# Kernel optimization log

Hardware: AMD Instinct MI355X
Metric: run time of the kernel (lower is better)

The kernel has to match this reference:

```python
import jax, jax.numpy as jnp
import numpy as np
from jax import lax

K = 3
PAD = 1

def setup_inputs() -> dict:
    key = jax.random.key(0)
    ks = jax.random.split(key, 5)
    B, C, H, W, O = 4, 128, 128, 128, 256
    x = jax.random.normal(ks[0], (B, C, H, W), dtype=jnp.float32)
    w_off = jax.random.normal(ks[1], (3 * K * K, C, K, K), dtype=jnp.float32) * 0.05
    b_off = jnp.zeros((3 * K * K,), dtype=jnp.float32)
    w_dw = jax.random.normal(ks[2], (C, 1, K, K), dtype=jnp.float32) * 0.2
    b_dw = jnp.zeros((C,), dtype=jnp.float32)
    w_pw = jax.random.normal(ks[3], (O, C), dtype=jnp.float32) * (1.0 / np.sqrt(C))
    b_pw = jnp.zeros((O,), dtype=jnp.float32)
    return {"x": x, "w_off": w_off, "b_off": b_off, "w_dw": w_dw,
            "b_dw": b_dw, "w_pw": w_pw, "b_pw": b_pw}

def _dcn_forward(x, w_off, b_off, w_dw, b_dw, w_pw, b_pw):
    B, C, H, W = x.shape
    K2 = K * K
    # offset/mask conv (stride 1, pad 1) -> [B, 3*K*K, H, W]
    om = lax.conv_general_dilated(
        x, w_off, window_strides=(1, 1), padding=[(PAD, PAD), (PAD, PAD)],
        dimension_numbers=("NCHW", "OIHW", "NCHW")) + b_off[None, :, None, None]
    off = om[:, : 2 * K2]                      # [B, 2*K2, H, W]
    mask = jax.nn.sigmoid(om[:, 2 * K2:])      # [B, K2, H, W]
    dy = off[:, 0::2]                          # [B, K2, H, W] (y offsets)
    dx = off[:, 1::2]                          # [B, K2, H, W] (x offsets)
    # base sampling grid per kernel tap
    ky, kx = jnp.meshgrid(jnp.arange(K), jnp.arange(K), indexing="ij")
    ky = (ky.reshape(-1) - PAD).astype(x.dtype)   # [K2]
    kx = (kx.reshape(-1) - PAD).astype(x.dtype)
    py = jnp.arange(H, dtype=x.dtype)[None, None, :, None] + ky[None, :, None, None] + dy
    px = jnp.arange(W, dtype=x.dtype)[None, None, None, :] + kx[None, :, None, None] + dx
    y0 = jnp.floor(py); x0 = jnp.floor(px)
    wy = py - y0;       wx = px - x0

    def gather(yc, xc):
        # yc, xc: [B, K2, H, W] float corner coords; zero outside bounds
        valid = ((yc >= 0) & (yc < H) & (xc >= 0) & (xc < W)).astype(x.dtype)
        yi = jnp.clip(yc, 0, H - 1).astype(jnp.int32)
        xi = jnp.clip(xc, 0, W - 1).astype(jnp.int32)
        idx = yi * W + xi                       # [B, K2, H, W]
        def per_b(xb, ib):
            # xb: [C, H, W]; ib: [K2, H, W] -> [C, K2, H, W]
            return jnp.take(xb.reshape(C, -1), ib.reshape(-1), axis=1).reshape(C, K2, H, W)
        v = jax.vmap(per_b)(x, idx)             # [B, C, K2, H, W]
        return v * valid[:, None]

    val = (gather(y0, x0) * ((1 - wy) * (1 - wx))[:, None]
           + gather(y0, x0 + 1) * ((1 - wy) * wx)[:, None]
           + gather(y0 + 1, x0) * (wy * (1 - wx))[:, None]
           + gather(y0 + 1, x0 + 1) * (wy * wx)[:, None])  # [B, C, K2, H, W]
    val = val * mask[:, None]
    # depthwise deformable conv: per-channel K2 weights
    wk = w_dw.reshape(C, K2)
    out = jnp.einsum("bckhw,ck->bchw", val, wk) + b_dw[None, :, None, None]
    # pointwise 1x1 conv
    out = jnp.einsum("bchw,oc->bohw", out, w_pw) + b_pw[None, :, None, None]
    return out

def reference(x, w_off, b_off, w_dw, b_dw, w_pw, b_pw):
    return _dcn_forward(x, w_off, b_off, w_dw, b_dw, w_pw, b_pw)
```

## Files before the change

kernel.cpp:

```cpp
#include <hip/hip_runtime.h>
#include <hip/hip_bf16.h>
#include <math.h>

#define BB 4
#define CC 128
#define HH 128
#define WW 128
#define OO 256
#define HWP 16384

typedef __attribute__((ext_vector_type(8))) _Float16 half8;
typedef __attribute__((ext_vector_type(2))) _Float16 half2t;
typedef __attribute__((ext_vector_type(4))) float floatx4;

__device__ inline half2t u2h2(unsigned int u) {
  union { unsigned int i; half2t h; } z; z.i = u; return z.h;
}
__device__ inline unsigned short f2h_bits(float f) {
  union { _Float16 h; unsigned short s; } z; z.h = (_Float16)f; return z.s;
}

__global__ __launch_bounds__(256) void k_transpose(const float* __restrict__ x,
                                                   const float* __restrict__ w_off,
                                                   const float* __restrict__ w_pw,
                                                   unsigned int* __restrict__ xh32,
                                                   _Float16* __restrict__ Ah,
                                                   _Float16* __restrict__ Apw) {
  int tid = threadIdx.x;
  if (blockIdx.z == 4) {
    int e = (blockIdx.x * 128 + blockIdx.y) * 256 + tid;
    if (e < 144 * 32 * 8) {
      int kblk = e >> 8;
      int o = (e >> 3) & 31;
      int j = e & 7;
      int k = kblk * 8 + j;
      int t = k >> 7, c = k & 127;
      float w = (o < 27) ? w_off[(o * CC + c) * 9 + t] : 0.0f;
      Ah[e] = (_Float16)w;
    }
    int e2 = e - 144 * 32 * 8;
    if (e2 >= 0 && e2 < 16 * 256 * 8) {
      int cblk = e2 >> 11;
      int o = (e2 >> 3) & 255;
      int j = e2 & 7;
      Apw[e2] = (_Float16)w_pw[o * CC + cblk * 8 + j];
    }
    return;
  }
  __shared__ float tile[64][65];
  int wt = blockIdx.x & 1;
  int ct = blockIdx.x >> 1;
  int h = blockIdx.y, b = blockIdx.z;
  int tw = tid & 63;
  int tc = tid >> 6;
#pragma unroll
  for (int i = 0; i < 16; i++) {
    int c = ct * 64 + i * 4 + tc;
    tile[i * 4 + tc][tw] = x[((b * CC + c) * HH + h) * WW + wt * 64 + tw];
  }
  __syncthreads();
  int cp = tid & 31;
  int wq = tid >> 5;
#pragma unroll
  for (int i = 0; i < 8; i++) {
    int wp = i * 8 + wq;
    int w = wt * 64 + wp;
    unsigned short h0 = f2h_bits(tile[cp * 2][wp]);
    unsigned short h1 = f2h_bits(tile[cp * 2 + 1][wp]);
    int idx2 = (((b * HH + h) * WW + w) * CC + ct * 64 + cp * 2) >> 1;
    xh32[idx2] = (unsigned int)h0 | ((unsigned int)h1 << 16);
  }
}

__global__ __launch_bounds__(256) void k_offconv_mfma(
    const _Float16* __restrict__ xh, const _Float16* __restrict__ Ah,
    const float* __restrict__ b_off, float* __restrict__ om) {
  int bid = blockIdx.x;
  int xcd = bid & 7, r = bid >> 3;
  int b = r >> 4;
  int h = xcd * 16 + (r & 15);
  int tid = threadIdx.x;
  int wv = tid >> 6, lane = tid & 63;
  int w0 = wv * 32;
  int n16 = lane & 15, quad = lane >> 4;

  floatx4 acc[2][2] = {};
  half8 zz = {};

  for (int t = 0; t < 9; t++) {
    int dy = t / 3 - 1, dx = t % 3 - 1;
    int hs = h + dy;
    bool hok = ((unsigned)hs < HH);
    int hsc = min(max(hs, 0), HH - 1);
    int wA = w0 + n16 + dx;
    int wB = wA + 16;
    bool okA = hok && ((unsigned)wA < WW);
    bool okB = hok && ((unsigned)wB < WW);
    int wAc = min(max(wA, 0), WW - 1);
    int wBc = min(max(wB, 0), WW - 1);
    size_t offA = (size_t)((b * HH + hsc) * WW + wAc) * CC + quad * 8;
    size_t offB = (size_t)((b * HH + hsc) * WW + wBc) * CC + quad * 8;
#pragma unroll
    for (int cs = 0; cs < 4; cs++) {
      int co = cs * 32;
      half8 bhA = *(const half8*)(xh + offA + co);
      half8 bhB = *(const half8*)(xh + offB + co);
      bhA = okA ? bhA : zz;
      bhB = okB ? bhB : zz;
      int kblk = t * 16 + cs * 4 + quad;
      const _Float16* pa = Ah + (size_t)kblk * 256 + n16 * 8;
      half8 a0 = *(const half8*)pa;
      half8 a1 = *(const half8*)(pa + 128);
      acc[0][0] = __builtin_amdgcn_mfma_f32_16x16x32_f16(a0, bhA, acc[0][0], 0, 0, 0);
      acc[1][0] = __builtin_amdgcn_mfma_f32_16x16x32_f16(a1, bhA, acc[1][0], 0, 0, 0);
      acc[0][1] = __builtin_amdgcn_mfma_f32_16x16x32_f16(a0, bhB, acc[0][1], 0, 0, 0);
      acc[1][1] = __builtin_amdgcn_mfma_f32_16x16x32_f16(a1, bhB, acc[1][1], 0, 0, 0);
    }
  }
#pragma unroll
  for (int mt = 0; mt < 2; mt++) {
#pragma unroll
    for (int reg = 0; reg < 4; reg++) {
      int o = mt * 16 + quad * 4 + reg;
      if (o < 27) {
        float bo = b_off[o];
#pragma unroll
        for (int nf = 0; nf < 2; nf++) {
          int w = w0 + nf * 16 + n16;
          om[((size_t)(b * 27 + o) << 14) + (h << 7) + w] = acc[mt][nf][reg] + bo;
        }
      }
    }
  }
}

__global__ __launch_bounds__(256) void k_sample(const unsigned short* __restrict__ xh,
                                                const float* __restrict__ om,
                                                const float* __restrict__ w_dw,
                                                const float* __restrict__ b_dw,
                                                unsigned short* __restrict__ out1h) {
  __shared__ int s_base[8][9], s_dxs[8][9], s_dys[8][9];
  __shared__ unsigned int s_wp[8][9][2];
  int tid = threadIdx.x;
  int bid = blockIdx.x;
  int n0 = ((bid & 7) * 1024 + (bid >> 3)) * 8;
  if (tid < 72) {
    int pix = tid / 9, k = tid - pix * 9;
    int n = n0 + pix;
    int b = n >> 14, rem = n & 16383;
    int h = rem >> 7, w = rem & 127;
    const float* op = om + b * 27 * HWP + rem;
    float dy = op[(2 * k) * HWP];
    float dx = op[(2 * k + 1) * HWP];
    float mv = op[(18 + k) * HWP];
    mv = 1.0f / (1.0f + __expf(-mv));
    float py = (float)(h + k / 3 - 1) + dy;
    float px = (float)(w + k % 3 - 1) + dx;
    float y0f = floorf(py), x0f = floorf(px);
    float wy = py - y0f, wx = px - x0f;
    int y0 = (int)y0f, x0 = (int)x0f;
    int y1 = y0 + 1, x1 = x0 + 1;
    float v00 = (y0 >= 0 && y0 < HH && x0 >= 0 && x0 < WW) ? 1.f : 0.f;
    float v01 = (y0 >= 0 && y0 < HH && x1 >= 0 && x1 < WW) ? 1.f : 0.f;
    float v10 = (y1 >= 0 && y1 < HH && x0 >= 0 && x0 < WW) ? 1.f : 0.f;
    float v11 = (y1 >= 0 && y1 < HH && x1 >= 0 && x1 < WW) ? 1.f : 0.f;
    int y0c = min(max(y0, 0), HH - 1), y1c = min(max(y1, 0), HH - 1);
    int x0c = min(max(x0, 0), WW - 1), x1c = min(max(x1, 0), WW - 1);
    s_base[pix][k] = ((b * HH + y0c) * WW + x0c) * CC;
    s_dxs[pix][k] = (x1c - x0c) * CC;
    s_dys[pix][k] = (y1c - y0c) * WW * CC;
    float w00 = (1.f - wy) * (1.f - wx) * mv * v00;
    float w01 = (1.f - wy) * wx * mv * v01;
    float w10 = wy * (1.f - wx) * mv * v10;
    float w11 = wy * wx * mv * v11;
    s_wp[pix][k][0] = (unsigned int)f2h_bits(w00) | ((unsigned int)f2h_bits(w01) << 16);
    s_wp[pix][k][1] = (unsigned int)f2h_bits(w10) | ((unsigned int)f2h_bits(w11) << 16);
  }
  __syncthreads();
  int wv = tid >> 6, lane = tid & 63;
  int pix = wv * 2 + (lane >> 5);
  int cl = lane & 31;
  int c0 = cl * 4;
  int n = n0 + pix;

  float4 wk4[9];
#pragma unroll
  for (int i = 0; i < 9; i++) wk4[i] = *(const float4*)(w_dw + c0 * 9 + i * 4);
  const float* wkf = (const float*)wk4;

  float acc0 = 0.f, acc1 = 0.f, acc2v = 0.f, acc3 = 0.f;
#pragma unroll
  for (int k = 0; k < 9; k++) {
    int base = s_base[pix][k] + c0;
    int dxs = s_dxs[pix][k], dys = s_dys[pix][k];
    uint2 a00 = *(const uint2*)(xh + base);
    uint2 a01 = *(const uint2*)(xh + base + dxs);
    uint2 a10 = *(const uint2*)(xh + base + dys);
    uint2 a11 = *(const uint2*)(xh + base + dys + dxs);
    half2t wt = u2h2(s_wp[pix][k][0]);
    half2t wb = u2h2(s_wp[pix][k][1]);
    unsigned int t0 = __builtin_amdgcn_perm(a01.x, a00.x, 0x05040100u);
    unsigned int t1 = __builtin_amdgcn_perm(a01.x, a00.x, 0x07060302u);
    unsigned int t2 = __builtin_amdgcn_perm(a01.y, a00.y, 0x05040100u);
    unsigned int t3 = __builtin_amdgcn_perm(a01.y, a00.y, 0x07060302u);
    unsigned int b0 = __builtin_amdgcn_perm(a11.x, a10.x, 0x05040100u);
    unsigned int b1 = __builtin_amdgcn_perm(a11.x, a10.x, 0x07060302u);
    unsigned int b2 = __builtin_amdgcn_perm(a11.y, a10.y, 0x05040100u);
    unsigned int b3 = __builtin_amdgcn_perm(a11.y, a10.y, 0x07060302u);
    float v0 = __builtin_amdgcn_fdot2(u2h2(b0), wb, __builtin_amdgcn_fdot2(u2h2(t0), wt, 0.f, false), false);
    float v1 = __builtin_amdgcn_fdot2(u2h2(b1), wb, __builtin_amdgcn_fdot2(u2h2(t1), wt, 0.f, false), false);
    float v2 = __builtin_amdgcn_fdot2(u2h2(b2), wb, __builtin_amdgcn_fdot2(u2h2(t2), wt, 0.f, false), false);
    float v3 = __builtin_amdgcn_fdot2(u2h2(b3), wb, __builtin_amdgcn_fdot2(u2h2(t3), wt, 0.f, false), false);
    acc0 = fmaf(v0, wkf[0 * 9 + k], acc0);
    acc1 = fmaf(v1, wkf[1 * 9 + k], acc1);
    acc2v = fmaf(v2, wkf[2 * 9 + k], acc2v);
    acc3 = fmaf(v3, wkf[3 * 9 + k], acc3);
  }
  float4 bd = *(const float4*)(b_dw + c0);
  acc0 += bd.x; acc1 += bd.y; acc2v += bd.z; acc3 += bd.w;
  ushort4 ov;
  ov.x = f2h_bits(acc0);
  ov.y = f2h_bits(acc1);
  ov.z = f2h_bits(acc2v);
  ov.w = f2h_bits(acc3);
  *(ushort4*)(out1h + (size_t)n * CC + c0) = ov;
}

__global__ __launch_bounds__(256) void k_pw_mfma(const _Float16* __restrict__ Apw,
                                                 const _Float16* __restrict__ out1h,
                                                 const float* __restrict__ bpw,
                                                 float* __restrict__ out) {
  int bid = blockIdx.x;
  int n0 = ((bid & 7) * 128 + (bid >> 3)) * 64;
  int tid = threadIdx.x;
  int wv = tid >> 6, lane = tid & 63;
  int n16 = lane & 15, quad = lane >> 4;
  int obase = wv * 64;

  floatx4 acc[4][4] = {};
#pragma unroll
  for (int cs = 0; cs < 4; cs++) {
    half8 af[4], bf[4];
#pragma unroll
    for (int mf = 0; mf < 4; mf++) {
      const _Float16* pa = Apw + ((size_t)(cs * 4 + quad) * 256 + obase + mf * 16 + n16) * 8;
      af[mf] = *(const half8*)pa;
    }
#pragma unroll
    for (int nf = 0; nf < 4; nf++) {
      const _Float16* pb = out1h + (size_t)(n0 + nf * 16 + n16) * CC + cs * 32 + quad * 8;
      bf[nf] = *(const half8*)pb;
    }
#pragma unroll
    for (int mf = 0; mf < 4; mf++)
#pragma unroll
      for (int nf = 0; nf < 4; nf++)
        acc[mf][nf] = __builtin_amdgcn_mfma_f32_16x16x32_f16(af[mf], bf[nf], acc[mf][nf], 0, 0, 0);
  }
  int b = n0 >> 14;
#pragma unroll
  for (int mf = 0; mf < 4; mf++) {
#pragma unroll
    for (int reg = 0; reg < 4; reg++) {
      int o = obase + mf * 16 + quad * 4 + reg;
      float bo = bpw[o];
#pragma unroll
      for (int nf = 0; nf < 4; nf++) {
        int n = n0 + nf * 16 + n16;
        int hw = n & 16383;
        out[((size_t)(b * OO + o) << 14) + hw] = acc[mf][nf][reg] + bo;
      }
    }
  }
}

extern "C" void kernel_launch(void* const* d_in, const int* in_sizes, int n_in,
                              void* d_out, int out_size, void* d_ws, size_t ws_size,
                              hipStream_t stream) {
  const float* x     = (const float*)d_in[0];
  const float* w_off = (const float*)d_in[1];
  const float* b_off = (const float*)d_in[2];
  const float* w_dw  = (const float*)d_in[3];
  const float* b_dw  = (const float*)d_in[4];
  const float* w_pw  = (const float*)d_in[5];
  const float* b_pw  = (const float*)d_in[6];
  float* out = (float*)d_out;
  float* ws  = (float*)d_ws;

  _Float16* xh = (_Float16*)out;

  float* om = ws;
  _Float16* out1h = (_Float16*)(ws + 1769472);
  _Float16* Ah = (_Float16*)(ws + 5963776);
  _Float16* Apw = Ah + 36864;

  k_transpose<<<dim3(4, 128, 5), 256, 0, stream>>>(x, w_off, w_pw,
                                                   (unsigned int*)xh, Ah, Apw);
  k_offconv_mfma<<<512, 256, 0, stream>>>(xh, Ah, b_off, om);
  k_sample<<<8192, 256, 0, stream>>>((const unsigned short*)xh, om, w_dw, b_dw,
                                     (unsigned short*)out1h);
  k_pw_mfma<<<1024, 256, 0, stream>>>(Apw, out1h, b_pw, out);
}
```

Before: 196.1 us.

## Store offset-conv output pixel-major and stage depthwise weights in LDS

```diff
diff --git a/kernel.cpp b/kernel.cpp
--- a/kernel.cpp
+++ b/kernel.cpp
@@ -117,6 +117,7 @@
       acc[1][1] = __builtin_amdgcn_mfma_f32_16x16x32_f16(a1, bhB, acc[1][1], 0, 0, 0);
     }
   }
+  int nbase = (b << 14) + (h << 7);
 #pragma unroll
   for (int mt = 0; mt < 2; mt++) {
 #pragma unroll
@@ -127,32 +128,36 @@
 #pragma unroll
         for (int nf = 0; nf < 2; nf++) {
           int w = w0 + nf * 16 + n16;
-          om[((size_t)(b * 27 + o) << 14) + (h << 7) + w] = acc[mt][nf][reg] + bo;
+          om[((size_t)(nbase + w) << 5) + o] = acc[mt][nf][reg] + bo;
         }
       }
     }
   }
 }
 
-__global__ __launch_bounds__(256) void k_sample(const unsigned short* __restrict__ xh,
-                                                const float* __restrict__ om,
-                                                const float* __restrict__ w_dw,
-                                                const float* __restrict__ b_dw,
-                                                unsigned short* __restrict__ out1h) {
+__global__ __launch_bounds__(256, 4) void k_sample(const unsigned short* __restrict__ xh,
+                                                   const float* __restrict__ om,
+                                                   const float* __restrict__ w_dw,
+                                                   const float* __restrict__ b_dw,
+                                                   unsigned short* __restrict__ out1h) {
   __shared__ int s_base[8][9], s_dxs[8][9], s_dys[8][9];
   __shared__ unsigned int s_wp[8][9][2];
+  __shared__ float s_wk[9][128];
   int tid = threadIdx.x;
   int bid = blockIdx.x;
   int n0 = ((bid & 7) * 1024 + (bid >> 3)) * 8;
+
+  for (int i = tid; i < 1152; i += 256) s_wk[i % 9][i / 9] = w_dw[i];
+
   if (tid < 72) {
     int pix = tid / 9, k = tid - pix * 9;
     int n = n0 + pix;
     int b = n >> 14, rem = n & 16383;
     int h = rem >> 7, w = rem & 127;
-    const float* op = om + b * 27 * HWP + rem;
-    float dy = op[(2 * k) * HWP];
-    float dx = op[(2 * k + 1) * HWP];
-    float mv = op[(18 + k) * HWP];
+    const float* op = om + ((size_t)n << 5);
+    float dy = op[2 * k];
+    float dx = op[2 * k + 1];
+    float mv = op[18 + k];
     mv = 1.0f / (1.0f + __expf(-mv));
     float py = (float)(h + k / 3 - 1) + dy;
     float px = (float)(w + k % 3 - 1) + dx;
@@ -183,11 +188,6 @@
   int c0 = cl * 4;
   int n = n0 + pix;
 
-  float4 wk4[9];
-#pragma unroll
-  for (int i = 0; i < 9; i++) wk4[i] = *(const float4*)(w_dw + c0 * 9 + i * 4);
-  const float* wkf = (const float*)wk4;
-
   float acc0 = 0.f, acc1 = 0.f, acc2v = 0.f, acc3 = 0.f;
 #pragma unroll
   for (int k = 0; k < 9; k++) {
@@ -211,10 +211,11 @@
     float v1 = __builtin_amdgcn_fdot2(u2h2(b1), wb, __builtin_amdgcn_fdot2(u2h2(t1), wt, 0.f, false), false);
     float v2 = __builtin_amdgcn_fdot2(u2h2(b2), wb, __builtin_amdgcn_fdot2(u2h2(t2), wt, 0.f, false), false);
     float v3 = __builtin_amdgcn_fdot2(u2h2(b3), wb, __builtin_amdgcn_fdot2(u2h2(t3), wt, 0.f, false), false);
-    acc0 = fmaf(v0, wkf[0 * 9 + k], acc0);
-    acc1 = fmaf(v1, wkf[1 * 9 + k], acc1);
-    acc2v = fmaf(v2, wkf[2 * 9 + k], acc2v);
-    acc3 = fmaf(v3, wkf[3 * 9 + k], acc3);
+    float4 wv4 = *(const float4*)&s_wk[k][c0];
+    acc0 = fmaf(v0, wv4.x, acc0);
+    acc1 = fmaf(v1, wv4.y, acc1);
+    acc2v = fmaf(v2, wv4.z, acc2v);
+    acc3 = fmaf(v3, wv4.w, acc3);
   }
   float4 bd = *(const float4*)(b_dw + c0);
   acc0 += bd.x; acc1 += bd.y; acc2v += bd.z; acc3 += bd.w;
@@ -288,10 +289,10 @@
   float* ws  = (float*)d_ws;
 
   _Float16* xh = (_Float16*)out;
-
-  float* om = ws;
-  _Float16* out1h = (_Float16*)(ws + 1769472);
-  _Float16* Ah = (_Float16*)(ws + 5963776);
+  float* om = out + 4194304;
+
+  _Float16* out1h = (_Float16*)ws;
+  _Float16* Ah = (_Float16*)(ws + 4194304);
   _Float16* Apw = Ah + 36864;
 
   k_transpose<<<dim3(4, 128, 5), 256, 0, stream>>>(x, w_off, w_pw,
```

New measurement: 187.7 us. -4.3%, faster.
